# Kernel tuning notes

Measured on AMD Instinct MI355X. Metric: run time of the kernel, lower is better.

## Reference

```python
import jax, jax.numpy as jnp
import numpy as np

B, S, D, H = 2, 2048, 1024, 16
HD = D // H
SCALE = HD ** -0.5

def setup_inputs() -> dict:
    key = jax.random.key(0)
    ks = jax.random.split(key, 3)
    x = jax.random.normal(ks[0], (B, S, D), dtype=jnp.float32)
    Wqkv = jax.random.normal(ks[1], (D, 3 * D), dtype=jnp.float32) * (D ** -0.5)
    bqkv = jnp.zeros((3 * D,), dtype=jnp.float32)
    Wproj = jax.random.normal(ks[2], (D, D), dtype=jnp.float32) * (D ** -0.5)
    bproj = jnp.zeros((D,), dtype=jnp.float32)
    return {"x": x, "Wqkv": Wqkv, "bqkv": bqkv, "Wproj": Wproj, "bproj": bproj}

def reference(x, Wqkv, bqkv, Wproj, bproj):
    b, s, d = x.shape
    qkv = x @ Wqkv + bqkv                       # (b, s, 3d)
    qkv = qkv.reshape(b, s, 3, H, HD)
    q, k, v = (qkv[:, :, 0], qkv[:, :, 1], qkv[:, :, 2])  # (b, s, h, hd)
    # scores: (b, h, s, s)
    attn = jnp.einsum('bqhd,bkhd->bhqk', q, k) * SCALE
    attn = jax.nn.softmax(attn, axis=-1)
    out = jnp.einsum('bhqk,bkhd->bqhd', attn, v).reshape(b, s, d)
    out = out @ Wproj + bproj
    return out
```

## Files before the change

### kernel.cpp

```cpp
#include <hip/hip_runtime.h>

typedef __attribute__((ext_vector_type(8))) short bf16x8;
typedef __attribute__((ext_vector_type(4))) float f32x4;
typedef __attribute__((ext_vector_type(16))) float f32x16;
typedef unsigned short u16;
typedef unsigned int u32;

#define MFMA16(a,b,c) __builtin_amdgcn_mfma_f32_16x16x32_bf16((a),(b),(c),0,0,0)
#define MFMA32(a,b,c) __builtin_amdgcn_mfma_f32_32x32x16_bf16((a),(b),(c),0,0,0)

#if __has_builtin(__builtin_amdgcn_exp2f)
#define EXP2(x) __builtin_amdgcn_exp2f(x)
#else
#define EXP2(x) __expf((x) * 0.6931471805599453f)
#endif

__device__ __forceinline__ u16 f2bf(float f) {
  u32 u = __builtin_bit_cast(u32, f);
  u += 0x7FFFu + ((u >> 16) & 1u);
  return (u16)(u >> 16);
}

__device__ __forceinline__ u32 cvtpk(float lo, float hi) {
  u32 r;
  asm("v_cvt_pk_bf16_f32 %0, %1, %2" : "=v"(r) : "v"(lo), "v"(hi));
  return r;
}

__device__ __forceinline__ void gload16(const u16* g, u16* l) {
  __builtin_amdgcn_global_load_lds(
      (const __attribute__((address_space(1))) u32*)(const void*)g,
      (__attribute__((address_space(3))) u32*)(void*)l, 16, 0, 0);
}

__device__ __forceinline__ bf16x8 ldsfrag(const u16* lds, int row, int chunk) {
  return *(const bf16x8*)(lds + row * 64 + ((chunk ^ (row & 7)) << 3));
}

__global__ __launch_bounds__(256) void convert_x(const float* __restrict__ in,
                                                 u16* __restrict__ out, int n4) {
  int i = blockIdx.x * blockDim.x + threadIdx.x;
  int stride = gridDim.x * blockDim.x;
  for (; i < n4; i += stride) {
    float4 v = ((const float4*)in)[i];
    u32 lo = (u32)f2bf(v.x) | ((u32)f2bf(v.y) << 16);
    u32 hi = (u32)f2bf(v.z) | ((u32)f2bf(v.w) << 16);
    uint2 pv; pv.x = lo; pv.y = hi;
    ((uint2*)out)[i] = pv;
  }
}

__global__ __launch_bounds__(256) void transpose_w(const float* __restrict__ in,
                                                   u16* __restrict__ out,
                                                   int R, int C) {
  __shared__ float t[32][33];
  int c0 = blockIdx.x * 32, r0 = blockIdx.y * 32;
  int tc = threadIdx.x & 31, tr = threadIdx.x >> 5;
#pragma unroll
  for (int j = 0; j < 4; ++j) {
    int r = tr + j * 8;
    t[r][tc] = in[(size_t)(r0 + r) * C + c0 + tc];
  }
  __syncthreads();
#pragma unroll
  for (int j = 0; j < 4; ++j) {
    int cc = tr + j * 8;
    out[(size_t)(c0 + cc) * R + r0 + tc] = f2bf(t[tc][cc]);
  }
}

template <int MODE>
__global__ __launch_bounds__(256) void gemm_k(
    const u16* __restrict__ A, const u16* __restrict__ Bt,
    const float* __restrict__ bias,
    u16* __restrict__ Qo, u16* __restrict__ Ko, u16* __restrict__ Vt,
    float* __restrict__ Of) {
  __shared__ alignas(16) u16 As[2][128 * 32];
  __shared__ alignas(16) u16 Bs[2][128 * 32];
  const int tid = threadIdx.x;
  const int wid = tid >> 6, lane = tid & 63;
  const int g = lane >> 4, lr = lane & 15;
  const int m0 = blockIdx.y * 128, n0 = blockIdx.x * 128;
  const int wr = (wid >> 1) * 64, wc = (wid & 1) * 64;

  f32x4 acc[4][4];
#pragma unroll
  for (int i = 0; i < 4; ++i)
#pragma unroll
    for (int j = 0; j < 4; ++j) acc[i][j] = (f32x4){0.f, 0.f, 0.f, 0.f};

  const u16* Ab = A + (size_t)m0 * 1024;
  const u16* Bb = Bt + (size_t)n0 * 1024;

  const int srow = tid >> 2, sc = tid & 3;
  auto stage = [&](int buf, int kt) {
#pragma unroll
    for (int i = 0; i < 2; ++i) {
      int s = tid + i * 256;
      int row = srow + i * 64, c = sc;
      gload16(Ab + (size_t)row * 1024 + kt + c * 8, As[buf] + s * 8);
      gload16(Bb + (size_t)row * 1024 + kt + c * 8, Bs[buf] + s * 8);
    }
  };

  stage(0, 0);
  __syncthreads();
  int cur = 0;
  for (int kt = 0; kt < 1024; kt += 32) {
    if (kt + 32 < 1024) stage(cur ^ 1, kt + 32);
    bf16x8 af[4], bfr[4];
#pragma unroll
    for (int i = 0; i < 4; ++i)
      af[i] = *(const bf16x8*)(As[cur] + (wr + i * 16 + lr) * 32 + g * 8);
#pragma unroll
    for (int j = 0; j < 4; ++j)
      bfr[j] = *(const bf16x8*)(Bs[cur] + (wc + j * 16 + lr) * 32 + g * 8);
    __builtin_amdgcn_s_setprio(1);
#pragma unroll
    for (int i = 0; i < 4; ++i)
#pragma unroll
      for (int j = 0; j < 4; ++j)
        acc[i][j] = MFMA16(af[i], bfr[j], acc[i][j]);
    __builtin_amdgcn_s_setprio(0);
    __syncthreads();
    cur ^= 1;
  }

  if constexpr (MODE == 1) {
#pragma unroll
    for (int i = 0; i < 4; ++i) {
      int row = m0 + wr + i * 16 + g * 4;
#pragma unroll
      for (int j = 0; j < 4; ++j) {
        int col = n0 + wc + j * 16 + lr;
        float bv = bias[col];
#pragma unroll
        for (int r = 0; r < 4; ++r)
          Of[(size_t)(row + r) * 1024 + col] = acc[i][j][r] + bv;
      }
    }
  } else {
    const int sel = n0 >> 10;
#pragma unroll
    for (int i = 0; i < 4; ++i) {
      int row = m0 + wr + i * 16 + g * 4;
      int b = row >> 11, s = row & 2047;
#pragma unroll
      for (int j = 0; j < 4; ++j) {
        int col = n0 + wc + j * 16 + lr;
        float bv = bias[col];
        int nn = col & 1023;
        int h = nn >> 6, hd = nn & 63;
        if (sel == 2) {
          u16 pk[4];
#pragma unroll
          for (int r = 0; r < 4; ++r) pk[r] = f2bf(acc[i][j][r] + bv);
          uint2 pv;
          pv.x = (u32)pk[0] | ((u32)pk[1] << 16);
          pv.y = (u32)pk[2] | ((u32)pk[3] << 16);
          *(uint2*)(Vt + (size_t)((b * 16 + h) * 64 + hd) * 2048 + s) = pv;
        } else {
          u16* dst = (sel == 0) ? Qo : Ko;
#pragma unroll
          for (int r = 0; r < 4; ++r)
            dst[(size_t)((b * 16 + h) * 2048 + s + r) * 64 + hd] =
                f2bf(acc[i][j][r] + bv);
        }
      }
    }
  }
}

__global__ __launch_bounds__(256, 2) void attn_k(const u16* __restrict__ Q,
                                                 const u16* __restrict__ K,
                                                 const u16* __restrict__ Vt,
                                                 u16* __restrict__ O) {
  __shared__ alignas(16) u16 Ks[2 * 64 * 64];
  __shared__ alignas(16) u16 Vs[2 * 64 * 64];
  __shared__ alignas(16) u32 Ps[4 * 32 * 32];
  const int tid = threadIdx.x;
  const int wid = tid >> 6, lane = tid & 63;
  const int l31 = lane & 31, b5 = lane >> 5;
  const int bh = blockIdx.y;
  const u16* Qh = Q + (size_t)bh * 2048 * 64;
  const u16* Kh = K + (size_t)bh * 2048 * 64;
  const u16* Vh = Vt + (size_t)bh * 64 * 2048;

#pragma unroll
  for (int i = 0; i < 2; ++i) {
    int s = tid + i * 256;
    int row = s >> 3, c = (s & 7) ^ (row & 7);
    gload16(Kh + row * 64 + c * 8, Ks + s * 8);
    gload16(Vh + row * 2048 + c * 8, Vs + s * 8);
  }

  const int qbase = blockIdx.x * 128 + wid * 32;
  const u16* qp = Qh + (size_t)(qbase + l31) * 64 + b5 * 8;
  bf16x8 qf[4];
#pragma unroll
  for (int c = 0; c < 4; ++c) qf[c] = *(const bf16x8*)(qp + 16 * c);
  __syncthreads();

  u32* pw = Ps + wid * 1024 + l31 * 32;
  const int swz = (l31 & 7) << 2;

  f32x16 accO0, accO1;
#pragma unroll
  for (int r = 0; r < 16; ++r) { accO0[r] = 0.f; accO1[r] = 0.f; }
  float mraw = -1e30f;
  float mC = 0.f;
  float lsum = 0.f;

  const float C2 = 0.125f * 1.44269504088896f;

  for (int t = 0; t < 32; ++t) {
    const u16* Kc = Ks + (t & 1) * 4096;
    const u16* Vc = Vs + (t & 1) * 4096;
    if (t < 31) {
      int kvn = (t + 1) * 64;
      u16* Kn = Ks + ((t + 1) & 1) * 4096;
      u16* Vn = Vs + ((t + 1) & 1) * 4096;
#pragma unroll
      for (int i = 0; i < 2; ++i) {
        int s = tid + i * 256;
        int row = s >> 3, c = (s & 7) ^ (row & 7);
        gload16(Kh + (kvn + row) * 64 + c * 8, Kn + s * 8);
        gload16(Vh + row * 2048 + kvn + c * 8, Vn + s * 8);
      }
    }

    f32x16 s0, s1;
#pragma unroll
    for (int r = 0; r < 16; ++r) { s0[r] = 0.f; s1[r] = 0.f; }
    __builtin_amdgcn_s_setprio(1);
#pragma unroll
    for (int c = 0; c < 4; ++c) {
      bf16x8 k0 = ldsfrag(Kc, l31, 2 * c + b5);
      bf16x8 k1 = ldsfrag(Kc, 32 + l31, 2 * c + b5);
      s0 = MFMA32(k0, qf[c], s0);
      s1 = MFMA32(k1, qf[c], s1);
    }
    __builtin_amdgcn_s_setprio(0);

    float rmax;
    {
      float a0 = fmaxf(fmaxf(s0[0], s0[1]), fmaxf(s0[2], s0[3]));
      float a1 = fmaxf(fmaxf(s0[4], s0[5]), fmaxf(s0[6], s0[7]));
      float a2 = fmaxf(fmaxf(s0[8], s0[9]), fmaxf(s0[10], s0[11]));
      float a3 = fmaxf(fmaxf(s0[12], s0[13]), fmaxf(s0[14], s0[15]));
      float b0 = fmaxf(fmaxf(s1[0], s1[1]), fmaxf(s1[2], s1[3]));
      float b1 = fmaxf(fmaxf(s1[4], s1[5]), fmaxf(s1[6], s1[7]));
      float b2 = fmaxf(fmaxf(s1[8], s1[9]), fmaxf(s1[10], s1[11]));
      float b3 = fmaxf(fmaxf(s1[12], s1[13]), fmaxf(s1[14], s1[15]));
      rmax = fmaxf(fmaxf(fmaxf(a0, a1), fmaxf(a2, a3)),
                   fmaxf(fmaxf(b0, b1), fmaxf(b2, b3)));
    }
    rmax = fmaxf(rmax, __shfl_xor(rmax, 32));

    if (__any(rmax > mraw + 64.f)) {
      float mn = fmaxf(mraw, rmax);
      float al = EXP2((mraw - mn) * C2);
      mraw = mn;
      mC = mn * C2;
      lsum *= al;
#pragma unroll
      for (int r = 0; r < 16; ++r) {
        float ar = __shfl(al, (r & 3) + 8 * (r >> 2) + 4 * b5);
        accO0[r] *= ar;
        accO1[r] *= ar;
      }
    }

    u32 w0[8], w1[8];
#pragma unroll
    for (int i = 0; i < 8; ++i) {
      float p0 = EXP2(__builtin_fmaf(s0[2 * i], C2, -mC));
      float p1 = EXP2(__builtin_fmaf(s0[2 * i + 1], C2, -mC));
      float p2 = EXP2(__builtin_fmaf(s1[2 * i], C2, -mC));
      float p3 = EXP2(__builtin_fmaf(s1[2 * i + 1], C2, -mC));
      lsum += (p0 + p1) + (p2 + p3);
      w0[i] = cvtpk(p0, p1);
      w1[i] = cvtpk(p2, p3);
    }
#pragma unroll
    for (int j = 0; j < 4; ++j) {
      uint2 a; a.x = w0[2 * j]; a.y = w0[2 * j + 1];
      uint2 b; b.x = w1[2 * j]; b.y = w1[2 * j + 1];
      *(uint2*)(pw + ((4 * j + 2 * b5) ^ swz)) = a;
      *(uint2*)(pw + ((16 + 4 * j + 2 * b5) ^ swz)) = b;
    }

    __builtin_amdgcn_s_setprio(1);
#pragma unroll
    for (int c = 0; c < 4; ++c) {
      bf16x8 pf = *(const bf16x8*)(pw + ((8 * c + 4 * b5) ^ swz));
      bf16x8 v0 = ldsfrag(Vc, l31, 2 * c + b5);
      bf16x8 v1 = ldsfrag(Vc, 32 + l31, 2 * c + b5);
      accO0 = MFMA32(pf, v0, accO0);
      accO1 = MFMA32(pf, v1, accO1);
    }
    __builtin_amdgcn_s_setprio(0);
    __syncthreads();
  }

  float ls = lsum + __shfl_xor(lsum, 32);
  float inv = 1.f / ls;
  const int b = bh >> 4, h = bh & 15;
#pragma unroll
  for (int r = 0; r < 16; ++r) {
    float ir = __shfl(inv, (r & 3) + 8 * (r >> 2) + 4 * b5);
    int qr = qbase + (r & 3) + 8 * (r >> 2) + 4 * b5;
    size_t rowoff = (size_t)(b * 2048 + qr) * 1024 + h * 64;
    O[rowoff + l31] = f2bf(accO0[r] * ir);
    O[rowoff + 32 + l31] = f2bf(accO1[r] * ir);
  }
}

extern "C" void kernel_launch(void* const* d_in, const int* in_sizes, int n_in,
                              void* d_out, int out_size, void* d_ws, size_t ws_size,
                              hipStream_t stream) {
  (void)in_sizes; (void)n_in; (void)out_size; (void)ws_size;
  const float* x = (const float*)d_in[0];
  const float* Wqkv = (const float*)d_in[1];
  const float* bqkv = (const float*)d_in[2];
  const float* Wproj = (const float*)d_in[3];
  const float* bproj = (const float*)d_in[4];
  float* out = (float*)d_out;

  char* ws = (char*)d_ws;
  size_t off = 0;
  auto alloc = [&](size_t bytes) {
    void* p = ws + off;
    off += (bytes + 255) & ~(size_t)255;
    return p;
  };
  u16* xb     = (u16*)alloc((size_t)4096 * 1024 * 2);
  u16* Wqkvt  = (u16*)alloc((size_t)3072 * 1024 * 2);
  u16* Wprojt = (u16*)alloc((size_t)1024 * 1024 * 2);
  u16* Qb     = (u16*)alloc((size_t)32 * 2048 * 64 * 2);
  u16* Kb     = (u16*)alloc((size_t)32 * 2048 * 64 * 2);
  u16* Vtb    = (u16*)alloc((size_t)32 * 64 * 2048 * 2);
  u16* AOb    = (u16*)alloc((size_t)4096 * 1024 * 2);

  convert_x<<<2048, 256, 0, stream>>>(x, xb, 4096 * 1024 / 4);
  transpose_w<<<dim3(96, 32), 256, 0, stream>>>(Wqkv, Wqkvt, 1024, 3072);
  transpose_w<<<dim3(32, 32), 256, 0, stream>>>(Wproj, Wprojt, 1024, 1024);
  gemm_k<0><<<dim3(24, 32), 256, 0, stream>>>(xb, Wqkvt, bqkv, Qb, Kb, Vtb, nullptr);
  attn_k<<<dim3(16, 32), 256, 0, stream>>>(Qb, Kb, Vtb, AOb);
  gemm_k<1><<<dim3(8, 32), 256, 0, stream>>>(AOb, Wprojt, bproj, nullptr, nullptr, nullptr, out);
}
```

Before: 132.9 us.

## Triple-buffer K/V tiles with vmcnt waits and remap attention blocks across XCDs

The attention kernel moves from double to triple buffering of K/V tiles in LDS. Loads are issued two tiles ahead, and explicit s_waitcnt vmcnt counts plus raw s_barrier replace __syncthreads, so global loads stay in flight across iterations. The grid is flattened to 1D and block indices are remapped so that neighbouring query tiles of the same head land on the same XCD, which should improve L2 reuse of K/V. Triple buffering adds about 16KB more LDS, which may lower occupancy, and the hand-counted vmcnt values depend on gload16 issuing exactly four memory ops per stage.

Result: no change. 131.0 us (-1.5%).

```diff
diff --git a/kernel.cpp b/kernel.cpp
--- a/kernel.cpp
+++ b/kernel.cpp
@@ -175,31 +175,37 @@
                                                  const u16* __restrict__ K,
                                                  const u16* __restrict__ Vt,
                                                  u16* __restrict__ O) {
-  __shared__ alignas(16) u16 Ks[2 * 64 * 64];
-  __shared__ alignas(16) u16 Vs[2 * 64 * 64];
-  __shared__ alignas(16) u32 Ps[4 * 32 * 32];
+  __shared__ alignas(16) u16 Ks[3][4096];
+  __shared__ alignas(16) u16 Vs[3][4096];
+  __shared__ alignas(16) u32 Ps[4 * 1024];
   const int tid = threadIdx.x;
   const int wid = tid >> 6, lane = tid & 63;
   const int l31 = lane & 31, b5 = lane >> 5;
-  const int bh = blockIdx.y;
+  const int p = blockIdx.x;
+  const int l = (p & 7) * 64 + (p >> 3);
+  const int qt = l & 15, bh = l >> 4;
   const u16* Qh = Q + (size_t)bh * 2048 * 64;
   const u16* Kh = K + (size_t)bh * 2048 * 64;
   const u16* Vh = Vt + (size_t)bh * 64 * 2048;
 
-#pragma unroll
-  for (int i = 0; i < 2; ++i) {
-    int s = tid + i * 256;
-    int row = s >> 3, c = (s & 7) ^ (row & 7);
-    gload16(Kh + row * 64 + c * 8, Ks + s * 8);
-    gload16(Vh + row * 2048 + c * 8, Vs + s * 8);
-  }
-
-  const int qbase = blockIdx.x * 128 + wid * 32;
+  const int qbase = qt * 128 + wid * 32;
   const u16* qp = Qh + (size_t)(qbase + l31) * 64 + b5 * 8;
   bf16x8 qf[4];
 #pragma unroll
   for (int c = 0; c < 4; ++c) qf[c] = *(const bf16x8*)(qp + 16 * c);
-  __syncthreads();
+  __builtin_amdgcn_sched_barrier(0);
+
+  auto stage = [&](int buf, int t) {
+#pragma unroll
+    for (int i = 0; i < 2; ++i) {
+      int s = tid + i * 256;
+      int row = s >> 3, c = (s & 7) ^ (row & 7);
+      gload16(Kh + (t * 64 + row) * 64 + c * 8, Ks[buf] + s * 8);
+      gload16(Vh + row * 2048 + t * 64 + c * 8, Vs[buf] + s * 8);
+    }
+  };
+  stage(0, 0);
+  stage(1, 1);
 
   u32* pw = Ps + wid * 1024 + l31 * 32;
   const int swz = (l31 & 7) << 2;
@@ -213,21 +219,21 @@
 
   const float C2 = 0.125f * 1.44269504088896f;
 
+  int cur = 0;
   for (int t = 0; t < 32; ++t) {
-    const u16* Kc = Ks + (t & 1) * 4096;
-    const u16* Vc = Vs + (t & 1) * 4096;
-    if (t < 31) {
-      int kvn = (t + 1) * 64;
-      u16* Kn = Ks + ((t + 1) & 1) * 4096;
-      u16* Vn = Vs + ((t + 1) & 1) * 4096;
-#pragma unroll
-      for (int i = 0; i < 2; ++i) {
-        int s = tid + i * 256;
-        int row = s >> 3, c = (s & 7) ^ (row & 7);
-        gload16(Kh + (kvn + row) * 64 + c * 8, Kn + s * 8);
-        gload16(Vh + row * 2048 + kvn + c * 8, Vn + s * 8);
-      }
-    }
+    if (t + 2 < 32) {
+      int nxt = cur + 2; if (nxt >= 3) nxt -= 3;
+      stage(nxt, t + 2);
+    }
+    if (t < 30)       asm volatile("s_waitcnt vmcnt(8)" ::: "memory");
+    else if (t == 30) asm volatile("s_waitcnt vmcnt(4)" ::: "memory");
+    else              asm volatile("s_waitcnt vmcnt(0)" ::: "memory");
+    __builtin_amdgcn_sched_barrier(0);
+    __builtin_amdgcn_s_barrier();
+    __builtin_amdgcn_sched_barrier(0);
+
+    const u16* Kc = Ks[cur];
+    const u16* Vc = Vs[cur];
 
     f32x16 s0, s1;
 #pragma unroll
@@ -300,7 +306,10 @@
       accO1 = MFMA32(pf, v1, accO1);
     }
     __builtin_amdgcn_s_setprio(0);
-    __syncthreads();
+
+    __builtin_amdgcn_s_barrier();
+    __builtin_amdgcn_sched_barrier(0);
+    cur += 1; if (cur >= 3) cur -= 3;
   }
 
   float ls = lsum + __shfl_xor(lsum, 32);
@@ -346,6 +355,6 @@
   transpose_w<<<dim3(96, 32), 256, 0, stream>>>(Wqkv, Wqkvt, 1024, 3072);
   transpose_w<<<dim3(32, 32), 256, 0, stream>>>(Wproj, Wprojt, 1024, 1024);
   gemm_k<0><<<dim3(24, 32), 256, 0, stream>>>(xb, Wqkvt, bqkv, Qb, Kb, Vtb, nullptr);
-  attn_k<<<dim3(16, 32), 256, 0, stream>>>(Qb, Kb, Vtb, AOb);
+  attn_k<<<512, 256, 0, stream>>>(Qb, Kb, Vtb, AOb);
   gemm_k<1><<<dim3(8, 32), 256, 0, stream>>>(AOb, Wprojt, bproj, nullptr, nullptr, nullptr, out);
 }
```
